# Optimization experiments

Hardware: AMD Instinct MI355X
Metric: run time of the kernel (lower is better)

## Reference

```python
import jax, jax.numpy as jnp
import numpy as np

B, NN, S = 8, 511, 512          # graphs, nodes, seq (= nodes + graph token)
D, H, DH = 768, 12, 64          # hidden, heads, head dim
FFN, L = 3072, 6                # ffn size, layers
VOCAB = 512

def layer_norm(x, s, b, eps=1e-5):
    m = x.mean(-1, keepdims=True)
    v = ((x - m) ** 2).mean(-1, keepdims=True)
    return (x - m) / jnp.sqrt(v + eps) * s + b

def setup_inputs() -> dict:
    key = jax.random.key(0)
    ks = jax.random.split(key, 24)
    std = 0.02 / np.sqrt(L)
    inp = {}
    inp['attn_bias'] = jax.random.normal(ks[0], (B, S, S), jnp.float32) * 0.1
    inp['spatial_pos'] = jax.random.normal(ks[1], (B, NN, NN, 1), jnp.float32)
    inp['x'] = jax.random.randint(ks[2], (B, NN, 1), 0, VOCAB)
    node_emb = jax.random.normal(ks[3], (VOCAB, D), jnp.float32) * 0.02
    inp['node_emb'] = node_emb.at[0].set(0.0)  # padding_idx=0
    inp['graph_token'] = jax.random.normal(ks[4], (1, D), jnp.float32) * 0.02
    inp['virt_dist'] = jax.random.normal(ks[5], (1, H), jnp.float32) * 0.02
    inp['sp_w1'] = jax.random.normal(ks[6], (1, 128), jnp.float32) * std
    inp['sp_b1'] = jnp.zeros((128,), jnp.float32)
    inp['sp_w2'] = jax.random.normal(ks[7], (128, H), jnp.float32) * std
    inp['sp_b2'] = jnp.zeros((H,), jnp.float32)
    inp['ln1_s'] = jnp.ones((L, D), jnp.float32)
    inp['ln1_b'] = jnp.zeros((L, D), jnp.float32)
    inp['wq'] = jax.random.normal(ks[8], (L, D, D), jnp.float32) * std
    inp['bq'] = jnp.zeros((L, D), jnp.float32)
    inp['wk'] = jax.random.normal(ks[9], (L, D, D), jnp.float32) * std
    inp['bk'] = jnp.zeros((L, D), jnp.float32)
    inp['wv'] = jax.random.normal(ks[10], (L, D, D), jnp.float32) * std
    inp['bv'] = jnp.zeros((L, D), jnp.float32)
    inp['wo'] = jax.random.normal(ks[11], (L, D, D), jnp.float32) * std
    inp['bo'] = jnp.zeros((L, D), jnp.float32)
    inp['ln2_s'] = jnp.ones((L, D), jnp.float32)
    inp['ln2_b'] = jnp.zeros((L, D), jnp.float32)
    inp['fw1'] = jax.random.normal(ks[12], (L, D, FFN), jnp.float32) * std
    inp['fb1'] = jnp.zeros((L, FFN), jnp.float32)
    inp['fw2'] = jax.random.normal(ks[13], (L, FFN, D), jnp.float32) * std
    inp['fb2'] = jnp.zeros((L, D), jnp.float32)
    inp['fln_s'] = jnp.ones((D,), jnp.float32)
    inp['fln_b'] = jnp.zeros((D,), jnp.float32)
    return inp

def reference(attn_bias, spatial_pos, x, node_emb, graph_token, virt_dist,
              sp_w1, sp_b1, sp_w2, sp_b2,
              ln1_s, ln1_b, wq, bq, wk, bk, wv, bv, wo, bo,
              ln2_s, ln2_b, fw1, fb1, fw2, fb2, fln_s, fln_b):
    scale = DH ** -0.5
    # node features: embedding lookup summed over per-node feature indices
    h = node_emb[x].sum(axis=-2)                                   # [B, NN, D]
    h = jnp.concatenate([jnp.broadcast_to(graph_token[None], (B, 1, D)), h], axis=1)  # [B, S, D]
    # structural bias: spatial-pos MLP -> per-head bias on node block
    sp_bias = (spatial_pos @ sp_w1 + sp_b1) @ sp_w2 + sp_b2        # [B, NN, NN, H]
    sp_bias = sp_bias.transpose(0, 3, 1, 2)                         # [B, H, NN, NN]
    # original adds attn_bias twice (clone-repeat, then + attn_bias.unsqueeze(1))
    bias = jnp.broadcast_to((2.0 * attn_bias)[:, None], (B, H, S, S))
    t = virt_dist.reshape(1, H, 1)
    bias = bias.at[:, :, 1:, 1:].add(sp_bias)
    bias = bias.at[:, :, 1:, 0].add(t)
    bias = bias.at[:, :, 0, :].add(t)
    for l in range(L):
        y = layer_norm(h, ln1_s[l], ln1_b[l])
        q = (y @ wq[l] + bq[l]).reshape(B, S, H, DH) * scale
        k = (y @ wk[l] + bk[l]).reshape(B, S, H, DH)
        v = (y @ wv[l] + bv[l]).reshape(B, S, H, DH)
        scores = jnp.einsum('bihd,bjhd->bhij', q, k) + bias
        att = jax.nn.softmax(scores, axis=-1)
        o = jnp.einsum('bhij,bjhd->bihd', att, v).reshape(B, S, D)
        h = h + (o @ wo[l] + bo[l])
        y = layer_norm(h, ln2_s[l], ln2_b[l])
        h = h + (jax.nn.gelu(y @ fw1[l] + fb1[l], approximate=False) @ fw2[l] + fb2[l])
    return layer_norm(h, fln_s, fln_b)
```

## Files before the change

kernel.cpp:

```cpp
#include <hip/hip_runtime.h>
#include <cstdint>
#include <cstddef>


typedef __attribute__((ext_vector_type(8))) short bf16x8;
typedef __attribute__((ext_vector_type(4))) short bf16x4;
typedef __attribute__((ext_vector_type(4))) float f32x4;
typedef __attribute__((ext_vector_type(4))) unsigned int u32x4;

static constexpr int D    = 768;
static constexpr int H    = 12;
static constexpr int S    = 512;
static constexpr int NN   = 511;
static constexpr int B    = 8;
static constexpr int FFN  = 3072;
static constexpr int ROWS = B * S;

__device__ __forceinline__ short f2b(float x) {
    union { float f; uint32_t u; } c; c.f = x;
    uint32_t r = (c.u + 0x7fffu + ((c.u >> 16) & 1u)) >> 16;
    return (short)(uint16_t)r;
}
__device__ __forceinline__ float b2f_lo(uint32_t u) {
    union { uint32_t u; float f; } c; c.u = u << 16; return c.f;
}
__device__ __forceinline__ float b2f_hi(uint32_t u) {
    union { uint32_t u; float f; } c; c.u = u & 0xffff0000u; return c.f;
}
__device__ __forceinline__ float gelu_f(float x) {
    return 0.5f * x * (1.0f + erff(x * 0.7071067811865476f));
}
__device__ __forceinline__ void gload16(const void* g, void* l) {
    __builtin_amdgcn_global_load_lds(
        (const __attribute__((address_space(1))) void*)g,
        (__attribute__((address_space(3))) void*)l, 16, 0, 0);
}

#if __has_builtin(__builtin_amdgcn_mfma_f32_16x16x16bf16_1k)
__device__ __forceinline__ f32x4 mfma16(bf16x4 a, bf16x4 b, f32x4 c) {
    return __builtin_amdgcn_mfma_f32_16x16x16bf16_1k(a, b, c, 0, 0, 0);
}
__device__ __forceinline__ void mfma16_fence(f32x4* o) { (void)o; }
#else
__device__ __forceinline__ f32x4 mfma16(bf16x4 a, bf16x4 b, f32x4 c) {
    asm volatile("s_nop 1\n\tv_mfma_f32_16x16x16_bf16 %0, %1, %2, %0"
                 : "+v"(c) : "v"(a), "v"(b));
    return c;
}
__device__ __forceinline__ void mfma16_fence(f32x4* o) {
    asm volatile("s_nop 7\n\ts_nop 7"
                 : "+v"(o[0]), "+v"(o[1]), "+v"(o[2]), "+v"(o[3]));
}
#endif

__global__ __launch_bounds__(256) void embed_kernel(
    const int* __restrict__ x, const float* __restrict__ emb,
    const float* __restrict__ gtok, float* __restrict__ h)
{
    int row = blockIdx.x;
    int b = row >> 9, s = row & (S - 1);
    const float* src = (s == 0) ? gtok : (emb + (size_t)x[b * NN + (s - 1)] * D);
    float* dst = h + (size_t)row * D;
    int t = threadIdx.x;
    dst[t]       = src[t];
    dst[t + 256] = src[t + 256];
    dst[t + 512] = src[t + 512];
}

__global__ void ac_kernel(const float* __restrict__ w1, const float* __restrict__ b1,
                          const float* __restrict__ w2, const float* __restrict__ b2,
                          float* __restrict__ ac)
{
    int h = threadIdx.x;
    if (h < H) {
        float a = 0.f, c = 0.f;
        for (int k = 0; k < 128; ++k) { a += w1[k] * w2[k * H + h]; c += b1[k] * w2[k * H + h]; }
        ac[h] = a; ac[16 + h] = c + b2[h];
    }
}

__global__ __launch_bounds__(256) void bias_pack_kernel(
    const float* __restrict__ ab, const float* __restrict__ sp,
    uint32_t* __restrict__ pb)
{
    int row = blockIdx.x;
    int b = row >> 9, i = row & 511;
    const float* abr = ab + (size_t)row * S;
    const float* spr = sp + ((size_t)b * NN + (i - 1)) * NN;
    uint32_t* out = pb + (size_t)row * S;
    #pragma unroll
    for (int jt = 0; jt < 2; ++jt) {
        int j = jt * 256 + threadIdx.x;
        float a2 = 2.f * abr[j];
        float spv = (i > 0 && j > 0) ? spr[j - 1] : 0.f;
        out[j] = (uint32_t)(uint16_t)f2b(a2) | ((uint32_t)(uint16_t)f2b(spv) << 16);
    }
}

__global__ __launch_bounds__(256) void wcvt_kernel(
    const float* __restrict__ wq, const float* __restrict__ wk,
    const float* __restrict__ wv, const float* __restrict__ wo,
    const float* __restrict__ f1, const float* __restrict__ f2,
    short* __restrict__ wqkvT, short* __restrict__ woT,
    short* __restrict__ f1T, short* __restrict__ f2T)
{
    int t = blockIdx.x;
    const float* in; short* out; int R, C, tr, tc;
    if (t < 432) {
        int which = t / 144, tt = t - which * 144;
        in = (which == 0) ? wq : ((which == 1) ? wk : wv);
        out = wqkvT + (size_t)which * 768 * 768;
        R = 768; C = 768; tr = tt / 12; tc = tt % 12;
    } else if (t < 576) {
        int tt = t - 432; in = wo; out = woT; R = 768; C = 768; tr = tt / 12; tc = tt % 12;
    } else if (t < 1152) {
        int tt = t - 576; in = f1; out = f1T; R = 768; C = 3072; tr = tt / 48; tc = tt % 48;
    } else {
        int tt = t - 1152; in = f2; out = f2T; R = 3072; C = 768; tr = tt / 12; tc = tt % 12;
    }
    int r0 = tr * 64, c0 = tc * 64;
    __shared__ short tile[64][65];
    int tid = threadIdx.x;
    #pragma unroll
    for (int i = 0; i < 16; ++i) {
        int e = i * 256 + tid; int r = e >> 6, c = e & 63;
        tile[r][c] = f2b(in[(size_t)(r0 + r) * C + c0 + c]);
    }
    __syncthreads();
    #pragma unroll
    for (int i = 0; i < 16; ++i) {
        int e = i * 256 + tid; int c = e >> 6, r = e & 63;
        out[(size_t)(c0 + c) * R + r0 + r] = tile[r][c];
    }
}

__global__ __launch_bounds__(256) void ln_kernel(
    const float* __restrict__ in, const float* __restrict__ sc,
    const float* __restrict__ bi, float* __restrict__ outF,
    short* __restrict__ outB)
{
    int row = blockIdx.x, t = threadIdx.x;
    const float* x = in + (size_t)row * D;
    float e0 = x[t], e1 = x[t + 256], e2 = x[t + 512];
    float s  = e0 + e1 + e2;
    float sq = e0 * e0 + e1 * e1 + e2 * e2;
    #pragma unroll
    for (int off = 1; off < 64; off <<= 1) { s += __shfl_xor(s, off); sq += __shfl_xor(sq, off); }
    __shared__ float red[8];
    int w = t >> 6, lane = t & 63;
    if (lane == 0) { red[w] = s; red[4 + w] = sq; }
    __syncthreads();
    s  = red[0] + red[1] + red[2] + red[3];
    sq = red[4] + red[5] + red[6] + red[7];
    float m   = s * (1.f / D);
    float inv = rsqrtf(sq * (1.f / D) - m * m + 1e-5f);
    float v0 = (e0 - m) * inv * sc[t]       + bi[t];
    float v1 = (e1 - m) * inv * sc[t + 256] + bi[t + 256];
    float v2 = (e2 - m) * inv * sc[t + 512] + bi[t + 512];
    if (outB) {
        short* o = outB + (size_t)row * D;
        o[t] = f2b(v0); o[t + 256] = f2b(v1); o[t + 512] = f2b(v2);
    } else {
        float* o = outF + (size_t)row * D;
        o[t] = v0; o[t + 256] = v1; o[t + 512] = v2;
    }
}

template<int BM>
__global__ __launch_bounds__(256) void gemm2(
    const short* __restrict__ A, const short* __restrict__ Wt,
    const float* __restrict__ Bb0, const float* __restrict__ Bb1, const float* __restrict__ Bb2,
    float* __restrict__ outF, const float* __restrict__ resid,
    short* __restrict__ outB,
    int K, int nper, int gx, float alpha0, int mode)
{
    constexpr int MR = BM / 32;
    __shared__ __align__(16) short As[2][BM * 32];
    __shared__ __align__(16) short Bs[2][128 * 32];
    int tid  = threadIdx.x;
    int lane = tid & 63;
    int w    = tid >> 6;

    int nwg = gridDim.x;
    int bid = blockIdx.x;
    int sid = (bid & 7) * (nwg >> 3) + (bid >> 3);
    int row0 = (sid % gx) * BM;
    int n0   = (sid / gx) * 128;

    int which = n0 / nper;
    int ncol0 = n0 - which * nper;
    const float* Bv = (which == 0) ? Bb0 : ((which == 1) ? Bb1 : Bb2);
    float alpha = (which == 0) ? alpha0 : 1.0f;

    int wr = (w >> 1) * (BM / 2);
    int wc = (w & 1) * 64;
    int fr = lane & 15;
    int kb8 = (lane >> 4) * 8;
    int sr = tid >> 2, skk = (tid & 3) * 8;

    f32x4 acc[MR][4] = {};

    auto stage = [&](int buf, int k0) {
        #pragma unroll
        for (int i = 0; i < BM / 64; ++i)
            gload16(A + (size_t)(row0 + i * 64 + sr) * K + k0 + skk,
                    (char*)&As[buf][0] + ((size_t)i * 256 + w * 64) * 16);
        #pragma unroll
        for (int i = 0; i < 2; ++i)
            gload16(Wt + (size_t)(n0 + i * 64 + sr) * K + k0 + skk,
                    (char*)&Bs[buf][0] + ((size_t)i * 256 + w * 64) * 16);
    };
    auto compute = [&](int buf) {
        bf16x8 af[MR], bfr[4];
        #pragma unroll
        for (int m = 0; m < MR; ++m) af[m]  = *(const bf16x8*)&As[buf][(wr + m * 16 + fr) * 32 + kb8];
        #pragma unroll
        for (int n = 0; n < 4; ++n) bfr[n] = *(const bf16x8*)&Bs[buf][(wc + n * 16 + fr) * 32 + kb8];
        #pragma unroll
        for (int m = 0; m < MR; ++m)
            #pragma unroll
            for (int n = 0; n < 4; ++n)
                acc[m][n] = __builtin_amdgcn_mfma_f32_16x16x32_bf16(af[m], bfr[n], acc[m][n], 0, 0, 0);
    };

    int nt = K >> 5;
    stage(0, 0);
    __syncthreads();
    int cur = 0;
    for (int t = 1; t < nt; ++t) {
        stage(cur ^ 1, t * 32);
        compute(cur);
        __syncthreads();
        cur ^= 1;
    }
    compute(cur);

    int rr = (lane >> 4) * 4;
    if (mode == 1) {
        short* base = outB + (size_t)which * ROWS * D;
        #pragma unroll
        for (int m = 0; m < MR; ++m) {
            int rowb = row0 + wr + m * 16 + rr;
            int b2 = rowb >> 9, s0 = rowb & 511;
            #pragma unroll
            for (int n = 0; n < 4; ++n) {
                int col = ncol0 + wc + n * 16 + fr;
                int h2 = col >> 6, d2 = col & 63;
                float bv = Bv[col];
                if (which == 2) {
                    bf16x4 pk;
                    #pragma unroll
                    for (int ri = 0; ri < 4; ++ri) pk[ri] = f2b(acc[m][n][ri] + bv);
                    *(bf16x4*)&base[(((size_t)b2 * H + h2) * 64 + d2) * 512 + s0] = pk;
                } else {
                    #pragma unroll
                    for (int ri = 0; ri < 4; ++ri)
                        base[(((size_t)b2 * H + h2) * 512 + (s0 + ri)) * 64 + d2] =
                            f2b((acc[m][n][ri] + bv) * alpha);
                }
            }
        }
        return;
    }

    #pragma unroll
    for (int m = 0; m < MR; ++m) {
        #pragma unroll
        for (int n = 0; n < 4; ++n) {
            int col  = ncol0 + wc + n * 16 + fr;
            float bv = Bv[col];
            #pragma unroll
            for (int ri = 0; ri < 4; ++ri) {
                int row = row0 + wr + m * 16 + rr + ri;
                size_t idx = (size_t)row * nper + col;
                float val = acc[m][n][ri] + bv;
                if (mode == 2) {
                    outB[idx] = f2b(gelu_f(val));
                } else {
                    outF[idx] = val + resid[idx];
                }
            }
        }
    }
}

__global__ __launch_bounds__(256) void attn_kernel(
    const short* __restrict__ qb, const short* __restrict__ kbuf,
    const short* __restrict__ vtb,
    const uint32_t* __restrict__ pb,
    const float* __restrict__ vd, const float* __restrict__ ac,
    short* __restrict__ o)
{
    __shared__ __align__(16) short Ks[2][128 * 64];
    __shared__ __align__(16) short Vs[2][64 * 128];
    int tid = threadIdx.x, lane = tid & 63, w = tid >> 6;
    int bid = blockIdx.x;
    int b    = bid & 7;
    int qblk = (bid >> 3) & 7;
    int hh   = bid >> 6;
    int fr = lane & 15, g16 = lane >> 4;
    int kb8 = g16 * 8, rr = g16 * 4;
    int i0 = qblk * 64 + w * 16;
    int i  = i0 + fr;

    const short* qp = qb   + ((size_t)(b * H + hh) * S) * 64;
    const short* kp = kbuf + ((size_t)(b * H + hh) * S) * 64;
    const short* vp = vtb  + ((size_t)(b * H + hh) * 64) * S;

    bf16x8 aq0 = *(const bf16x8*)&qp[(i0 + fr) * 64 + kb8];
    bf16x8 aq1 = *(const bf16x8*)&qp[(i0 + fr) * 64 + 32 + kb8];

    float Ah = ac[hh], Ch = ac[16 + hh], th = vd[hh];
    const uint32_t* pbb = pb + (size_t)b * S * S + (size_t)i * S;

    auto stageK = [&](int buf, int j0) {
        #pragma unroll
        for (int ii = 0; ii < 4; ++ii) {
            int U = ii * 256 + tid;
            int r = U >> 3;
            int ch = (U & 7) ^ (r & 7);
            gload16(kp + (size_t)(j0 + r) * 64 + ch * 8,
                    (char*)&Ks[buf][0] + ((size_t)ii * 256 + w * 64) * 16);
        }
    };
    auto stageV = [&](int buf, int j0) {
        #pragma unroll
        for (int ii = 0; ii < 4; ++ii) {
            int U = ii * 256 + tid;
            int d = U >> 4;
            int s8 = (2 * (U & 15)) ^ (d & 14);
            gload16(vp + (size_t)d * S + j0 + s8 * 4,
                    (char*)&Vs[buf][0] + ((size_t)ii * 256 + w * 64) * 16);
        }
    };

    float m_run = -3.0e38f, l_run = 0.f;
    f32x4 oacc[4] = {};

    stageK(0, 0);
    stageV(0, 0);
    __syncthreads();
    int buf = 0;
    #pragma unroll 1
    for (int t = 0; t < 4; ++t) {
        if (t < 3) { stageK(buf ^ 1, (t + 1) * 128); stageV(buf ^ 1, (t + 1) * 128); }
        f32x4 s[8];
        #pragma unroll
        for (int jt = 0; jt < 8; ++jt) {
            int jb = t * 8 + jt;
            u32x4 u = *(const u32x4*)&pbb[jb * 16 + rr];
            f32x4 c;
            #pragma unroll
            for (int ri = 0; ri < 4; ++ri) {
                int j = jb * 16 + rr + ri;
                float bias = b2f_lo(u[ri]);
                if (i > 0 && j > 0) bias += b2f_hi(u[ri]) * Ah + Ch;
                if (i == 0 || j == 0) bias += th;
                c[ri] = bias;
            }
            int r = jt * 16 + fr;
            const char* krow = (const char*)&Ks[buf][0] + r * 128;
            bf16x8 kf0 = *(const bf16x8*)(krow + ((g16 ^ (r & 7)) * 16));
            bf16x8 kf1 = *(const bf16x8*)(krow + (((g16 + 4) ^ (r & 7)) * 16));
            c = __builtin_amdgcn_mfma_f32_16x16x32_bf16(kf0, aq0, c, 0, 0, 0);
            s[jt] = __builtin_amdgcn_mfma_f32_16x16x32_bf16(kf1, aq1, c, 0, 0, 0);
        }
        float tm = s[0][0];
        #pragma unroll
        for (int jt = 0; jt < 8; ++jt)
            #pragma unroll
            for (int ri = 0; ri < 4; ++ri) tm = fmaxf(tm, s[jt][ri]);
        tm = fmaxf(tm, __shfl_xor(tm, 16));
        tm = fmaxf(tm, __shfl_xor(tm, 32));
        float mnew = fmaxf(m_run, tm);
        float scale = __expf(m_run - mnew);
        l_run *= scale;
        #pragma unroll
        for (int ri = 0; ri < 4; ++ri) {
            float scr = __shfl(scale, rr + ri);
            #pragma unroll
            for (int dt = 0; dt < 4; ++dt) oacc[dt][ri] *= scr;
        }
        #pragma unroll
        for (int jt = 0; jt < 8; ++jt)
            #pragma unroll
            for (int ri = 0; ri < 4; ++ri) {
                float p = __expf(s[jt][ri] - mnew);
                s[jt][ri] = p;
                l_run += p;
            }
        #pragma unroll
        for (int jt = 0; jt < 8; ++jt) {
            bf16x4 pa;
            #pragma unroll
            for (int ri = 0; ri < 4; ++ri) pa[ri] = f2b(s[jt][ri]);
            #pragma unroll
            for (int dt = 0; dt < 4; ++dt) {
                int d = dt * 16 + fr;
                const char* vrow = (const char*)&Vs[buf][0] + d * 256;
                bf16x4 vb = *(const bf16x4*)(vrow + (((jt * 4 + g16) ^ (d & 14)) * 8));
                oacc[dt] = mfma16(pa, vb, oacc[dt]);
            }
        }
        m_run = mnew;
        __syncthreads();
        buf ^= 1;
    }
    mfma16_fence(oacc);

    l_run += __shfl_xor(l_run, 16);
    l_run += __shfl_xor(l_run, 32);
    float invl = 1.f / l_run;
    #pragma unroll
    for (int ri = 0; ri < 4; ++ri) {
        float ivr = __shfl(invl, rr + ri);
        #pragma unroll
        for (int dt = 0; dt < 4; ++dt)
            o[((size_t)(b * S + i0 + rr + ri) * H + hh) * 64 + dt * 16 + fr] =
                f2b(oacc[dt][ri] * ivr);
    }
}

extern "C" void kernel_launch(void* const* d_in, const int* in_sizes, int n_in,
                              void* d_out, int out_size, void* d_ws, size_t ws_size,
                              hipStream_t stream)
{
    const float* attn_bias   = (const float*)d_in[0];
    const float* spatial_pos = (const float*)d_in[1];
    const int*   xx          = (const int*)d_in[2];
    const float* node_emb    = (const float*)d_in[3];
    const float* graph_token = (const float*)d_in[4];
    const float* virt_dist   = (const float*)d_in[5];
    const float* sp_w1 = (const float*)d_in[6];
    const float* sp_b1 = (const float*)d_in[7];
    const float* sp_w2 = (const float*)d_in[8];
    const float* sp_b2 = (const float*)d_in[9];
    const float* ln1_s = (const float*)d_in[10];
    const float* ln1_b = (const float*)d_in[11];
    const float* wq = (const float*)d_in[12];
    const float* bq = (const float*)d_in[13];
    const float* wk = (const float*)d_in[14];
    const float* bk = (const float*)d_in[15];
    const float* wv = (const float*)d_in[16];
    const float* bv = (const float*)d_in[17];
    const float* wo = (const float*)d_in[18];
    const float* bo = (const float*)d_in[19];
    const float* ln2_s = (const float*)d_in[20];
    const float* ln2_b = (const float*)d_in[21];
    const float* fw1 = (const float*)d_in[22];
    const float* fb1 = (const float*)d_in[23];
    const float* fw2 = (const float*)d_in[24];
    const float* fb2 = (const float*)d_in[25];
    const float* fln_s = (const float*)d_in[26];
    const float* fln_b = (const float*)d_in[27];

    float* wsf = (float*)d_ws;
    const size_t SZ = (size_t)ROWS * D;
    float* h   = wsf;
    float* acb = wsf + SZ;
    short* s16 = (short*)(wsf + SZ + 64);
    short* yob = s16;
    short* g16b = s16 + SZ;
    short* bfq = g16b + (size_t)ROWS * FFN;
    short* wqkvT = bfq + 3 * SZ;
    short* woT   = wqkvT + 2304 * 768;
    short* f1T   = woT + 768 * 768;
    short* f2T   = f1T + (size_t)3072 * 768;
    uint32_t* pbias = (uint32_t*)(f2T + (size_t)768 * 3072);

    embed_kernel<<<ROWS, 256, 0, stream>>>(xx, node_emb, graph_token, h);
    ac_kernel<<<1, 64, 0, stream>>>(sp_w1, sp_b1, sp_w2, sp_b2, acb);
    bias_pack_kernel<<<ROWS, 256, 0, stream>>>(attn_bias, spatial_pos, pbias);

    for (int l = 0; l < 6; ++l) {
        wcvt_kernel<<<1728, 256, 0, stream>>>(
            wq + (size_t)l * D * D, wk + (size_t)l * D * D, wv + (size_t)l * D * D,
            wo + (size_t)l * D * D, fw1 + (size_t)l * D * FFN, fw2 + (size_t)l * FFN * D,
            wqkvT, woT, f1T, f2T);
        ln_kernel<<<ROWS, 256, 0, stream>>>(h, ln1_s + l * D, ln1_b + l * D, nullptr, yob);
        gemm2<128><<<576, 256, 0, stream>>>(
            yob, wqkvT, bq + l * D, bk + l * D, bv + l * D,
            nullptr, nullptr, bfq, D, D, 32, 0.125f, 1);
        attn_kernel<<<B * H * 8, 256, 0, stream>>>(
            bfq, bfq + SZ, bfq + 2 * SZ, pbias, virt_dist, acb, yob);
        gemm2<64><<<384, 256, 0, stream>>>(
            yob, woT, bo + l * D, nullptr, nullptr,
            h, h, nullptr, D, D, 64, 1.0f, 0);
        ln_kernel<<<ROWS, 256, 0, stream>>>(h, ln2_s + l * D, ln2_b + l * D, nullptr, yob);
        gemm2<128><<<768, 256, 0, stream>>>(
            yob, f1T, fb1 + l * FFN, nullptr, nullptr,
            nullptr, nullptr, g16b, D, FFN, 32, 1.0f, 2);
        gemm2<64><<<384, 256, 0, stream>>>(
            g16b, f2T, fb2 + l * D, nullptr, nullptr,
            h, h, nullptr, FFN, D, 64, 1.0f, 0);
    }
    ln_kernel<<<ROWS, 256, 0, stream>>>(h, fln_s, fln_b, (float*)d_out, nullptr);
}
```

Measured before the change: 1.252 ms.

## Double GEMM K-tile to 64 with XOR-swizzled LDS layout

The gemm2 kernel now stages 64-wide K slices instead of 32 per double-buffered iteration, which halves the number of barriers and loop trips. To keep LDS reads free of bank conflicts at the 128-byte row pitch, 16-byte chunks are stored XOR-swizzled by row index and read back with the matching swizzle. LDS usage per block doubles, which may lower occupancy.

Measured after the change: 1.376 ms. +9.9%, slower.

```diff
diff --git a/kernel.cpp b/kernel.cpp
--- a/kernel.cpp
+++ b/kernel.cpp
@@ -175,8 +175,8 @@
     int K, int nper, int gx, float alpha0, int mode)
 {
     constexpr int MR = BM / 32;
-    __shared__ __align__(16) short As[2][BM * 32];
-    __shared__ __align__(16) short Bs[2][128 * 32];
+    __shared__ __align__(16) short As[2][BM * 64];
+    __shared__ __align__(16) short Bs[2][128 * 64];
     int tid  = threadIdx.x;
     int lane = tid & 63;
     int w    = tid >> 6;
@@ -195,47 +195,68 @@
     int wr = (w >> 1) * (BM / 2);
     int wc = (w & 1) * 64;
     int fr = lane & 15;
-    int kb8 = (lane >> 4) * 8;
-    int sr = tid >> 2, skk = (tid & 3) * 8;
+    int q4 = lane >> 4;
 
     f32x4 acc[MR][4] = {};
 
-    auto stage = [&](int buf, int k0) {
-        #pragma unroll
-        for (int i = 0; i < BM / 64; ++i)
-            gload16(A + (size_t)(row0 + i * 64 + sr) * K + k0 + skk,
-                    (char*)&As[buf][0] + ((size_t)i * 256 + w * 64) * 16);
-        #pragma unroll
-        for (int i = 0; i < 2; ++i)
-            gload16(Wt + (size_t)(n0 + i * 64 + sr) * K + k0 + skk,
-                    (char*)&Bs[buf][0] + ((size_t)i * 256 + w * 64) * 16);
+    auto stageA = [&](int buf, int k0) {
+        #pragma unroll
+        for (int ii = 0; ii < BM / 32; ++ii) {
+            int U = ii * 256 + tid;
+            int r = U >> 3;
+            int ch = (U & 7) ^ (r & 7);
+            gload16(A + (size_t)(row0 + r) * K + k0 + ch * 8,
+                    (char*)&As[buf][0] + ((size_t)ii * 256 + w * 64) * 16);
+        }
+    };
+    auto stageB = [&](int buf, int k0) {
+        #pragma unroll
+        for (int ii = 0; ii < 4; ++ii) {
+            int U = ii * 256 + tid;
+            int r = U >> 3;
+            int ch = (U & 7) ^ (r & 7);
+            gload16(Wt + (size_t)(n0 + r) * K + k0 + ch * 8,
+                    (char*)&Bs[buf][0] + ((size_t)ii * 256 + w * 64) * 16);
+        }
     };
     auto compute = [&](int buf) {
-        bf16x8 af[MR], bfr[4];
-        #pragma unroll
-        for (int m = 0; m < MR; ++m) af[m]  = *(const bf16x8*)&As[buf][(wr + m * 16 + fr) * 32 + kb8];
-        #pragma unroll
-        for (int n = 0; n < 4; ++n) bfr[n] = *(const bf16x8*)&Bs[buf][(wc + n * 16 + fr) * 32 + kb8];
-        #pragma unroll
-        for (int m = 0; m < MR; ++m)
-            #pragma unroll
-            for (int n = 0; n < 4; ++n)
-                acc[m][n] = __builtin_amdgcn_mfma_f32_16x16x32_bf16(af[m], bfr[n], acc[m][n], 0, 0, 0);
+        #pragma unroll
+        for (int s = 0; s < 2; ++s) {
+            bf16x8 af[MR], bfr[4];
+            #pragma unroll
+            for (int m = 0; m < MR; ++m) {
+                int r = wr + m * 16 + fr;
+                af[m] = *(const bf16x8*)((const char*)&As[buf][0]
+                        + (size_t)r * 128 + (((q4 + 4 * s) ^ (r & 7)) * 16));
+            }
+            #pragma unroll
+            for (int n = 0; n < 4; ++n) {
+                int r = wc + n * 16 + fr;
+                bfr[n] = *(const bf16x8*)((const char*)&Bs[buf][0]
+                        + (size_t)r * 128 + (((q4 + 4 * s) ^ (r & 7)) * 16));
+            }
+            #pragma unroll
+            for (int m = 0; m < MR; ++m)
+                #pragma unroll
+                for (int n = 0; n < 4; ++n)
+                    acc[m][n] = __builtin_amdgcn_mfma_f32_16x16x32_bf16(af[m], bfr[n], acc[m][n], 0, 0, 0);
+        }
     };
 
-    int nt = K >> 5;
-    stage(0, 0);
+    int nt = K >> 6;
+    stageA(0, 0); stageB(0, 0);
     __syncthreads();
     int cur = 0;
     for (int t = 1; t < nt; ++t) {
-        stage(cur ^ 1, t * 32);
+        stageA(cur ^ 1, t * 64);
+        stageB(cur ^ 1, t * 64);
         compute(cur);
         __syncthreads();
         cur ^= 1;
     }
     compute(cur);
 
-    int rr = (lane >> 4) * 4;
+    int rr = q4 * 4;
     if (mode == 1) {
         short* base = outB + (size_t)which * ROWS * D;
         #pragma unroll
```
